# Performance work log

Hardware: AMD Instinct MI355X
Metric: run time of the kernel (lower is better)

## Reference

```python
import jax, jax.numpy as jnp
import numpy as np

CURV_BOUNDS = (-2.0, 2.0)
THRESH = 0.01   # |k| below this -> Euclidean branch
EPS = 1e-5

B, S, D = 4, 2048, 512


def setup_inputs() -> dict:
    key = jax.random.key(0)
    ks = jax.random.split(key, 8)
    x = jax.random.normal(ks[0], (B, S, D), jnp.float32)
    sc = 1.0 / np.sqrt(D)  # ~ nn.Linear default init scale
    Wq = jax.random.uniform(ks[1], (D, D), jnp.float32, -sc, sc)
    bq = jax.random.uniform(ks[2], (D,), jnp.float32, -sc, sc)
    Wk = jax.random.uniform(ks[3], (D, D), jnp.float32, -sc, sc)
    bk = jax.random.uniform(ks[4], (D,), jnp.float32, -sc, sc)
    Wv = jax.random.uniform(ks[5], (D, D), jnp.float32, -sc, sc)
    bv = jax.random.uniform(ks[6], (D,), jnp.float32, -sc, sc)
    curvature_raw = jnp.float32(0.5)   # init_curvature
    temperature = jnp.float32(1.0)
    mask = jnp.triu(jnp.ones((S, S), dtype=bool), 1)  # causal: True = masked out
    return {"x": x, "Wq": Wq, "bq": bq, "Wk": Wk, "bk": bk, "Wv": Wv,
            "bv": bv, "curvature_raw": curvature_raw,
            "temperature": temperature, "mask": mask}


def _curvature(raw):
    k_min, k_max = CURV_BOUNDS
    return k_min + (k_max - k_min) * (jnp.tanh(raw) + 1.0) / 2.0


def _project(u, k):
    # project_to_manifold: identity (euclid), Poincare-ball clip (k<0), sphere renorm (k>0)
    n = jnp.sqrt(jnp.sum(u * u, axis=-1, keepdims=True) + 1e-12)
    absk = jnp.abs(k)
    sk = jnp.sqrt(jnp.maximum(absk, EPS))
    max_norm = (1.0 - 1e-3) / sk                      # ball radius 1/sqrt(|k|)
    u_hyp = u * jnp.minimum(1.0, max_norm / n)
    u_sph = u / (n * sk)                              # sphere radius 1/sqrt(k)
    return jnp.where(absk < THRESH, u, jnp.where(k < 0, u_hyp, u_sph))


def reference(x, Wq, bq, Wk, bk, Wv, bv, curvature_raw, temperature, mask):
    k = _curvature(curvature_raw)
    q = x @ Wq.T + bq
    kk = x @ Wk.T + bk
    v = x @ Wv.T + bv
    qm = _project(q, k)
    km = _project(kk, k)

    # pairwise quantities without materializing [B,S,S,D]
    dots = jnp.einsum('bid,bjd->bij', qm, km)         # [B,S,S]
    qn2 = jnp.sum(qm * qm, axis=-1)                   # [B,S]
    kn2 = jnp.sum(km * km, axis=-1)                   # [B,S]
    diff2 = jnp.maximum(qn2[:, :, None] + kn2[:, None, :] - 2.0 * dots, 0.0)

    absk = jnp.abs(k)
    sk = jnp.sqrt(jnp.maximum(absk, EPS))

    d_euc = jnp.sqrt(diff2 + 1e-12)
    # hyperbolic (Poincare ball, c=|k|): acosh(1 + 2c|x-y|^2 / ((1-c|x|^2)(1-c|y|^2))) / sqrt(c)
    denom = jnp.maximum((1.0 - absk * qn2)[:, :, None] * (1.0 - absk * kn2)[:, None, :], EPS)
    arg = 1.0 + 2.0 * absk * diff2 / denom
    d_hyp = jnp.arccosh(jnp.maximum(arg, 1.0 + 1e-7)) / sk
    # spherical (radius 1/sqrt(k)): arccos(k * <x,y>) / sqrt(k)
    cosang = jnp.clip(absk * dots, -1.0 + 1e-7, 1.0 - 1e-7)
    d_sph = jnp.arccos(cosang) / sk

    dist = jnp.where(absk < THRESH, d_euc, jnp.where(k < 0, d_hyp, d_sph))

    scores = -dist / (temperature + 1e-8)
    scores = jnp.where(mask[None, :, :], -jnp.inf, scores)
    attention = jax.nn.softmax(scores, axis=-1)       # [B,S,S]
    output = jnp.einsum('bij,bjd->bid', attention, v) # [B,S,D]
    return output, attention
```

## Files before the change

### kernel.cpp

```cpp
#include <hip/hip_runtime.h>
#include <hip/hip_bf16.h>
#include <math.h>

typedef unsigned short u16;
typedef float float4e __attribute__((ext_vector_type(4)));
typedef short short8 __attribute__((ext_vector_type(8)));
typedef unsigned short ushort8 __attribute__((ext_vector_type(8)));
typedef unsigned short u16x4 __attribute__((ext_vector_type(4)));

#define SEQ 2048
#define DIM 512
#define NB  4

__device__ __forceinline__ float bf2f(u16 h) {
    return __uint_as_float(((unsigned)h) << 16);
}
__device__ __forceinline__ u16 f2bf(float f) {
    __hip_bfloat16 h = __float2bfloat16(f);
    return *reinterpret_cast<u16*>(&h);
}
__device__ __forceinline__ float curv_of(float raw) {
    return -2.0f + 2.0f * (tanhf(raw) + 1.0f);
}
__device__ __forceinline__ void gl_lds16(const u16* g, u16* lds) {
    __builtin_amdgcn_global_load_lds(
        (const __attribute__((address_space(1))) unsigned int*)g,
        (__attribute__((address_space(3))) unsigned int*)lds, 16, 0, 0);
}

__global__ __launch_bounds__(256) void cvt_all_kernel(
    const float* __restrict__ x, const float* __restrict__ Wq,
    const float* __restrict__ Wk, const float* __restrict__ Wv,
    u16* __restrict__ x_bf, u16* __restrict__ Wcat,
    float* __restrict__ lsum, float* __restrict__ qn2r, float* __restrict__ kn2r)
{
    const int n_x = NB * SEQ * DIM, n_w = DIM * DIM;
    int gid = blockIdx.x * 256 + threadIdx.x;
    if (gid < NB * SEQ) { lsum[gid] = 0.f; qn2r[gid] = 0.f; kn2r[gid] = 0.f; }
    int i4 = gid * 4;
    if (i4 < n_x) {
        float4 v = *(const float4*)&x[i4];
        u16x4 h = {f2bf(v.x), f2bf(v.y), f2bf(v.z), f2bf(v.w)};
        *(u16x4*)&x_bf[i4] = h;
    } else if (i4 < n_x + 3 * n_w) {
        int j = i4 - n_x;
        const float* W = (j < n_w) ? Wq : (j < 2 * n_w ? Wk : Wv);
        int off = j % n_w;
        float4 v = *(const float4*)&W[off];
        u16x4 h = {f2bf(v.x), f2bf(v.y), f2bf(v.z), f2bf(v.w)};
        *(u16x4*)&Wcat[j] = h;
    }
}

__global__ __launch_bounds__(256, 2) void gemm_qkv_kernel(
    const u16* __restrict__ A, const u16* __restrict__ Bt,
    u16* __restrict__ qbuf, u16* __restrict__ kbuf, u16* __restrict__ vT,
    const float* __restrict__ bq, const float* __restrict__ bk, const float* __restrict__ bv,
    float* __restrict__ qn2r, float* __restrict__ kn2r)
{
    const int lda = 512, ldb = 512;
    int n = blockIdx.x;
    int xcd = n & 7, i = n >> 3;
    int bn = i % 12, bm = xcd + 8 * (i / 12);

    __shared__ __align__(16) u16 As[128 * 64];
    __shared__ __align__(16) u16 Bs[128 * 64];

    int t = threadIdx.x, wave = t >> 6, lane = t & 63;
    int wr = wave >> 1, wc = wave & 1;
    int lrow = lane & 15, quad = lane >> 4;
    int srow = lane >> 3, sc8 = lane & 7;

    const u16* Ab = A + (size_t)(bm * 128) * lda;
    const u16* Bb = Bt + (size_t)(bn * 128) * ldb;

    float4e acc[4][4];
#pragma unroll
    for (int i2 = 0; i2 < 4; i2++)
#pragma unroll
        for (int j = 0; j < 4; j++) acc[i2][j] = (float4e){0.f, 0.f, 0.f, 0.f};

    for (int kt = 0; kt < 8; ++kt) {
        int k0 = kt << 6;
        __syncthreads();
#pragma unroll
        for (int h = 0; h < 4; ++h) {
            int q = wave * 4 + h;
            int row = q * 8 + srow;
            int c = sc8 ^ (row & 7);
            gl_lds16(Ab + (size_t)row * lda + k0 + c * 8, &As[q * 512]);
            gl_lds16(Bb + (size_t)row * ldb + k0 + c * 8, &Bs[q * 512]);
        }
        __syncthreads();
#pragma unroll
        for (int kk = 0; kk < 2; ++kk) {
            short8 af[4], bfr[4];
#pragma unroll
            for (int im = 0; im < 4; im++) {
                int R = wr * 64 + im * 16 + lrow;
                af[im] = *(const short8*)&As[R * 64 + (((kk * 4 + quad) ^ (R & 7)) * 8)];
            }
#pragma unroll
            for (int in = 0; in < 4; in++) {
                int R = wc * 64 + in * 16 + lrow;
                bfr[in] = *(const short8*)&Bs[R * 64 + (((kk * 4 + quad) ^ (R & 7)) * 8)];
            }
#pragma unroll
            for (int im = 0; im < 4; im++)
#pragma unroll
                for (int in = 0; in < 4; in++)
                    acc[im][in] = __builtin_amdgcn_mfma_f32_16x16x32_bf16(af[im], bfr[in], acc[im][in], 0, 0, 0);
        }
    }

    int region = bn >> 2;
    float nsum[4][4];
#pragma unroll
    for (int im = 0; im < 4; im++)
#pragma unroll
        for (int r = 0; r < 4; r++) nsum[im][r] = 0.f;

#pragma unroll
    for (int in = 0; in < 4; in++) {
        int gj = bn * 128 + wc * 64 + in * 16 + lrow;
        float bias = (gj < 512) ? bq[gj] : (gj < 1024 ? bk[gj - 512] : bv[gj - 1024]);
#pragma unroll
        for (int im = 0; im < 4; im++) {
            int gi0 = bm * 128 + wr * 64 + im * 16 + quad * 4;
            u16x4 pack;
#pragma unroll
            for (int r = 0; r < 4; r++) {
                u16 hv = f2bf(acc[im][in][r] + bias);
                pack[r] = hv;
                if (region == 0) {
                    qbuf[(size_t)(gi0 + r) * 512 + gj] = hv;
                } else if (region == 1) {
                    kbuf[(size_t)(gi0 + r) * 512 + (gj - 512)] = hv;
                }
                if (region < 2) { float vv = bf2f(hv); nsum[im][r] += vv * vv; }
            }
            if (region == 2) {
                int bb = gi0 >> 11, s = gi0 & 2047;
                *(u16x4*)&vT[((size_t)bb * DIM + (gj - 1024)) * SEQ + s] = pack;
            }
        }
    }
    if (region < 2) {
        float* nrm = (region == 0) ? qn2r : kn2r;
#pragma unroll
        for (int im = 0; im < 4; im++)
#pragma unroll
            for (int r = 0; r < 4; r++) {
                float v = nsum[im][r];
                v += __shfl_xor(v, 1);
                v += __shfl_xor(v, 2);
                v += __shfl_xor(v, 4);
                v += __shfl_xor(v, 8);
                if (lrow == 0)
                    atomicAdd(&nrm[bm * 128 + wr * 64 + im * 16 + quad * 4 + r], v);
            }
    }
}

__global__ __launch_bounds__(256) void rownorm_kernel(
    const float* __restrict__ qn2r, const float* __restrict__ kn2r,
    float2* __restrict__ qpk, float2* __restrict__ kpk,
    const float* __restrict__ curvp)
{
    int i = blockIdx.x * 256 + threadIdx.x;
    float kv = curv_of(curvp[0]);
    float absk = fabsf(kv);
    float sk = sqrtf(fmaxf(absk, 1e-5f));
    bool euc = (absk < 0.01f);
    float mxn = (1.0f - 1e-3f) / sk;

    float qr = qn2r[i];
    float nq = sqrtf(qr + 1e-12f);
    float sq_ = euc ? 1.f : (kv < 0.f ? fminf(1.f, mxn / nq) : 1.f / (nq * sk));
    qpk[i] = make_float2(qr * sq_ * sq_, sq_);

    float kr = kn2r[i];
    float nk = sqrtf(kr + 1e-12f);
    float sk_ = euc ? 1.f : (kv < 0.f ? fminf(1.f, mxn / nk) : 1.f / (nk * sk));
    kpk[i] = make_float2(kr * sk_ * sk_, sk_);
}

__global__ __launch_bounds__(256, 2) void gemm_scores_kernel(
    const u16* __restrict__ qbuf, const u16* __restrict__ kbuf,
    u16* __restrict__ attnH, float* __restrict__ lsum,
    const float2* __restrict__ qpk, const float2* __restrict__ kpk,
    const float* __restrict__ curvp, const float* __restrict__ tempp)
{
    const int lda = 512, ldb = 512, ldc = SEQ;
    int n = blockIdx.x;
    int xcd = n & 7, i = n >> 3;
    int bn = i & 15;
    int strip = xcd + 8 * (i >> 4);
    int bm = strip & 15, b = strip >> 4;
    if (bn > bm) return;

    __shared__ __align__(16) u16 As[128 * 64];
    __shared__ __align__(16) u16 Bs[128 * 64];

    int t = threadIdx.x, wave = t >> 6, lane = t & 63;
    int wr = wave >> 1, wc = wave & 1;
    int lrow = lane & 15, quad = lane >> 4;
    int srow = lane >> 3, sc8 = lane & 7;

    const u16* Ab = qbuf + (size_t)(b * SEQ + bm * 128) * lda;
    const u16* Bb = kbuf + (size_t)(b * SEQ + bn * 128) * ldb;

    float4e acc[4][4];
#pragma unroll
    for (int i2 = 0; i2 < 4; i2++)
#pragma unroll
        for (int j = 0; j < 4; j++) acc[i2][j] = (float4e){0.f, 0.f, 0.f, 0.f};

    for (int kt = 0; kt < 8; ++kt) {
        int k0 = kt << 6;
        __syncthreads();
#pragma unroll
        for (int h = 0; h < 4; ++h) {
            int q = wave * 4 + h;
            int row = q * 8 + srow;
            int c = sc8 ^ (row & 7);
            gl_lds16(Ab + (size_t)row * lda + k0 + c * 8, &As[q * 512]);
            gl_lds16(Bb + (size_t)row * ldb + k0 + c * 8, &Bs[q * 512]);
        }
        __syncthreads();
#pragma unroll
        for (int kk = 0; kk < 2; ++kk) {
            short8 af[4], bfr[4];
#pragma unroll
            for (int im = 0; im < 4; im++) {
                int R = wr * 64 + im * 16 + lrow;
                af[im] = *(const short8*)&As[R * 64 + (((kk * 4 + quad) ^ (R & 7)) * 8)];
            }
#pragma unroll
            for (int in = 0; in < 4; in++) {
                int R = wc * 64 + in * 16 + lrow;
                bfr[in] = *(const short8*)&Bs[R * 64 + (((kk * 4 + quad) ^ (R & 7)) * 8)];
            }
#pragma unroll
            for (int im = 0; im < 4; im++)
#pragma unroll
                for (int in = 0; in < 4; in++)
                    acc[im][in] = __builtin_amdgcn_mfma_f32_16x16x32_bf16(af[im], bfr[in], acc[im][in], 0, 0, 0);
        }
    }

    float kv = curv_of(curvp[0]);
    float absk = fabsf(kv);
    float sk = sqrtf(fmaxf(absk, 1e-5f));
    bool euc = (absk < 0.01f);
    float invT = 1.0f / (tempp[0] + 1e-8f);
    float Cexp = -1.4426950408889634f * invT;
    u16* Cb = attnH + (size_t)b * SEQ * SEQ;

    float2 kp[4];
#pragma unroll
    for (int in = 0; in < 4; in++)
        kp[in] = kpk[b * SEQ + bn * 128 + wc * 64 + in * 16 + lrow];

    float psum[4][4];
#pragma unroll
    for (int im = 0; im < 4; im++)
#pragma unroll
        for (int r = 0; r < 4; r++) psum[im][r] = 0.f;

#pragma unroll
    for (int im = 0; im < 4; im++) {
#pragma unroll
        for (int r = 0; r < 4; r++) {
            int gi = bm * 128 + wr * 64 + im * 16 + quad * 4 + r;
            float2 qp = qpk[b * SEQ + gi];
            float qn = qp.x;
#pragma unroll
            for (int in = 0; in < 4; in++) {
                int gj = bn * 128 + wc * 64 + in * 16 + lrow;
                float kn = kp[in].x;
                float dot = acc[im][in][r] * qp.y * kp[in].y;
                float diff2 = fmaxf(qn + kn - 2.f * dot, 0.f);
                float dist;
                if (euc) {
                    dist = sqrtf(diff2 + 1e-12f);
                } else if (kv < 0.f) {
                    float denom = fmaxf((1.f - absk * qn) * (1.f - absk * kn), 1e-5f);
                    float arg = fmaxf(1.f + 2.f * absk * diff2 / denom, 1.f + 1e-7f);
                    dist = acoshf(arg) / sk;
                } else {
                    float c = fminf(fmaxf(absk * dot, -1.f + 1e-7f), 1.f - 1e-7f);
                    dist = acosf(c) / sk;
                }
                float e = (gj <= gi) ? exp2f(dist * Cexp) : 0.f;
                Cb[(size_t)gi * ldc + gj] = f2bf(e);
                psum[im][r] += e;
            }
        }
    }
#pragma unroll
    for (int im = 0; im < 4; im++)
#pragma unroll
        for (int r = 0; r < 4; r++) {
            float v = psum[im][r];
            v += __shfl_xor(v, 1);
            v += __shfl_xor(v, 2);
            v += __shfl_xor(v, 4);
            v += __shfl_xor(v, 8);
            if (lrow == 0) {
                int gi = bm * 128 + wr * 64 + im * 16 + quad * 4 + r;
                atomicAdd(&lsum[b * SEQ + gi], v);
            }
        }
}

__global__ __launch_bounds__(256, 4) void gemm_pv_kernel(
    const u16* __restrict__ attnH, const u16* __restrict__ vT,
    float* __restrict__ out, float* __restrict__ attnF,
    const float* __restrict__ lsum)
{
    const int lda = SEQ, ldb = SEQ, ldc = DIM;
    int n = blockIdx.x;
    int xcd = n & 7, i = n >> 3;
    int bn = i & 7;
    int strip = xcd + 8 * (i >> 3);
    int bm = strip & 31, b = strip >> 5;

    __shared__ __align__(16) u16 As[64 * 64];
    __shared__ __align__(16) u16 Bs[64 * 64];

    int t = threadIdx.x, wave = t >> 6, lane = t & 63;
    int wr = wave >> 1, wc = wave & 1;
    int lrow = lane & 15, quad = lane >> 4;
    int srow = lane >> 3, sc = lane & 7;

    const u16* Ab = attnH + (size_t)b * SEQ * SEQ + (size_t)(bm * 64) * lda;
    const u16* Bb = vT + (size_t)b * DIM * SEQ + (size_t)(bn * 64) * ldb;
    float* attnFb = attnF + (size_t)b * SEQ * SEQ;

    {
        int r = t >> 2, c4 = t & 3;
        float4 z = (float4){0.f, 0.f, 0.f, 0.f};
        for (int kt = bm + 1; kt < 32; ++kt)
            if ((kt & 7) == bn) {
                float* dst = attnFb + (size_t)(bm * 64 + r) * SEQ + kt * 64 + c4 * 16;
                ((float4*)dst)[0] = z; ((float4*)dst)[1] = z;
                ((float4*)dst)[2] = z; ((float4*)dst)[3] = z;
            }
    }

    float4e acc[2][2];
#pragma unroll
    for (int i2 = 0; i2 < 2; i2++)
#pragma unroll
        for (int j = 0; j < 2; j++) acc[i2][j] = (float4e){0.f, 0.f, 0.f, 0.f};

    for (int kt = 0; kt <= bm; ++kt) {
        int k0 = kt << 6;
        __syncthreads();
#pragma unroll
        for (int h = 0; h < 2; ++h) {
            int q = wave * 2 + h;
            int row = q * 8 + srow;
            int c = sc ^ (row & 7);
            gl_lds16(Ab + (size_t)row * lda + k0 + c * 8, &As[q * 512]);
            gl_lds16(Bb + (size_t)row * ldb + k0 + c * 8, &Bs[q * 512]);
        }
        __syncthreads();
#pragma unroll
        for (int s = 0; s < 2; ++s) {
            short8 af[2], bfr[2];
#pragma unroll
            for (int im = 0; im < 2; im++) {
                int R = wr * 32 + im * 16 + lrow;
                af[im] = *(const short8*)&As[R * 64 + (((s * 4 + quad) ^ (R & 7)) * 8)];
            }
#pragma unroll
            for (int in = 0; in < 2; in++) {
                int R = wc * 32 + in * 16 + lrow;
                bfr[in] = *(const short8*)&Bs[R * 64 + (((s * 4 + quad) ^ (R & 7)) * 8)];
            }
#pragma unroll
            for (int im = 0; im < 2; im++)
#pragma unroll
                for (int in = 0; in < 2; in++)
                    acc[im][in] = __builtin_amdgcn_mfma_f32_16x16x32_bf16(af[im], bfr[in], acc[im][in], 0, 0, 0);
        }
        if ((kt & 7) == bn) {
            int r = t >> 2, c4 = t & 3;
            int gi = bm * 64 + r;
            float invl = 1.0f / lsum[b * SEQ + gi];
            const u16* src = &As[r * 64];
            int j0 = c4 * 2;
            ushort8 u0 = *(const ushort8*)&src[(j0 ^ (r & 7)) * 8];
            ushort8 u1 = *(const ushort8*)&src[((j0 + 1) ^ (r & 7)) * 8];
            float* dst = attnFb + (size_t)gi * SEQ + kt * 64 + c4 * 16;
            float4 f0 = {bf2f(u0[0]) * invl, bf2f(u0[1]) * invl, bf2f(u0[2]) * invl, bf2f(u0[3]) * invl};
            float4 f1 = {bf2f(u0[4]) * invl, bf2f(u0[5]) * invl, bf2f(u0[6]) * invl, bf2f(u0[7]) * invl};
            float4 f2 = {bf2f(u1[0]) * invl, bf2f(u1[1]) * invl, bf2f(u1[2]) * invl, bf2f(u1[3]) * invl};
            float4 f3 = {bf2f(u1[4]) * invl, bf2f(u1[5]) * invl, bf2f(u1[6]) * invl, bf2f(u1[7]) * invl};
            ((float4*)dst)[0] = f0; ((float4*)dst)[1] = f1;
            ((float4*)dst)[2] = f2; ((float4*)dst)[3] = f3;
        }
    }

    float* Cb = out + (size_t)b * SEQ * DIM;
#pragma unroll
    for (int im = 0; im < 2; im++)
#pragma unroll
        for (int r = 0; r < 4; r++) {
            int gi = bm * 64 + wr * 32 + im * 16 + quad * 4 + r;
            float invl = 1.0f / lsum[b * SEQ + gi];
#pragma unroll
            for (int in = 0; in < 2; in++) {
                int gd = bn * 64 + wc * 32 + in * 16 + lrow;
                Cb[(size_t)gi * ldc + gd] = acc[im][in][r] * invl;
            }
        }
}

extern "C" void kernel_launch(void* const* d_in, const int* in_sizes, int n_in,
                              void* d_out, int out_size, void* d_ws, size_t ws_size,
                              hipStream_t stream) {
    (void)in_sizes; (void)n_in; (void)out_size; (void)ws_size;

    const float* x    = (const float*)d_in[0];
    const float* Wq   = (const float*)d_in[1];
    const float* bq   = (const float*)d_in[2];
    const float* Wk   = (const float*)d_in[3];
    const float* bk   = (const float*)d_in[4];
    const float* Wv   = (const float*)d_in[5];
    const float* bv   = (const float*)d_in[6];
    const float* curv = (const float*)d_in[7];
    const float* temp = (const float*)d_in[8];

    float* out   = (float*)d_out;
    float* attnF = out + (size_t)NB * SEQ * DIM;

    char* ws = (char*)d_ws;
    u16*   x_bf  = (u16*)(ws + 0);
    u16*   Wcat  = (u16*)(ws + 8388608);
    u16*   attnH = (u16*)(ws + 0);
    u16*   qbuf  = (u16*)(ws + 33554432);
    u16*   kbuf  = (u16*)(ws + 41943040);
    u16*   vT    = (u16*)(ws + 50331648);
    float* qn2r  = (float*)(ws + 58720256);
    float* kn2r  = (float*)(ws + 58753024);
    float* lsum  = (float*)(ws + 58785792);
    float2* qpk  = (float2*)(ws + 58818560);
    float2* kpk  = (float2*)(ws + 58884096);

    {
        int n_tot = (NB * SEQ * DIM + 3 * DIM * DIM) / 4;
        cvt_all_kernel<<<(n_tot + 255) / 256, 256, 0, stream>>>(
            x, Wq, Wk, Wv, x_bf, Wcat, lsum, qn2r, kn2r);
    }

    gemm_qkv_kernel<<<768, 256, 0, stream>>>(
        x_bf, Wcat, qbuf, kbuf, vT, bq, bk, bv, qn2r, kn2r);

    rownorm_kernel<<<NB * SEQ / 256, 256, 0, stream>>>(qn2r, kn2r, qpk, kpk, curv);

    gemm_scores_kernel<<<1024, 256, 0, stream>>>(
        qbuf, kbuf, attnH, lsum, qpk, kpk, curv, temp);

    gemm_pv_kernel<<<1024, 256, 0, stream>>>(
        attnH, vT, out, attnF, lsum);
}
```

Measured before the change: 234.0 us.

## Double-buffer LDS tiles with async prefetch in all three GEMM kernels

Each GEMM kernel (QKV projection, scores, PV) now keeps two LDS buffers and issues the global-to-LDS loads for the next K tile before computing the current one. It waits on a partial vmcnt so the newest loads stay in flight, and syncs with explicit barriers. The aim is to hide global load latency behind MFMA work. In exchange LDS use doubles, which can lower occupancy for the launch_bounds(256,4) PV kernel. Correctness also now depends on the hand-set vmcnt values matching the number of loads issued per stage.

```diff
diff --git a/kernel.cpp b/kernel.cpp
--- a/kernel.cpp
+++ b/kernel.cpp
@@ -11,6 +11,9 @@
 #define SEQ 2048
 #define DIM 512
 #define NB  4
+
+#define VMCNT(n) asm volatile("s_waitcnt vmcnt(" #n ")" ::: "memory")
+#define BAR() __builtin_amdgcn_s_barrier()
 
 __device__ __forceinline__ float bf2f(u16 h) {
     return __uint_as_float(((unsigned)h) << 16);
@@ -63,8 +66,8 @@
     int xcd = n & 7, i = n >> 3;
     int bn = i % 12, bm = xcd + 8 * (i / 12);
 
-    __shared__ __align__(16) u16 As[128 * 64];
-    __shared__ __align__(16) u16 Bs[128 * 64];
+    __shared__ __align__(16) u16 As[2][128 * 64];
+    __shared__ __align__(16) u16 Bs[2][128 * 64];
 
     int t = threadIdx.x, wave = t >> 6, lane = t & 63;
     int wr = wave >> 1, wc = wave & 1;
@@ -74,36 +77,42 @@
     const u16* Ab = A + (size_t)(bm * 128) * lda;
     const u16* Bb = Bt + (size_t)(bn * 128) * ldb;
 
-    float4e acc[4][4];
-#pragma unroll
-    for (int i2 = 0; i2 < 4; i2++)
-#pragma unroll
-        for (int j = 0; j < 4; j++) acc[i2][j] = (float4e){0.f, 0.f, 0.f, 0.f};
-
-    for (int kt = 0; kt < 8; ++kt) {
+    auto stage = [&](int buf, int kt) {
         int k0 = kt << 6;
-        __syncthreads();
 #pragma unroll
         for (int h = 0; h < 4; ++h) {
             int q = wave * 4 + h;
             int row = q * 8 + srow;
             int c = sc8 ^ (row & 7);
-            gl_lds16(Ab + (size_t)row * lda + k0 + c * 8, &As[q * 512]);
-            gl_lds16(Bb + (size_t)row * ldb + k0 + c * 8, &Bs[q * 512]);
-        }
-        __syncthreads();
+            gl_lds16(Ab + (size_t)row * lda + k0 + c * 8, &As[buf][q * 512]);
+            gl_lds16(Bb + (size_t)row * ldb + k0 + c * 8, &Bs[buf][q * 512]);
+        }
+    };
+
+    float4e acc[4][4];
+#pragma unroll
+    for (int i2 = 0; i2 < 4; i2++)
+#pragma unroll
+        for (int j = 0; j < 4; j++) acc[i2][j] = (float4e){0.f, 0.f, 0.f, 0.f};
+
+    stage(0, 0);
+    for (int kt = 0; kt < 8; ++kt) {
+        int cur = kt & 1;
+        if (kt + 1 < 8) { stage(cur ^ 1, kt + 1); VMCNT(8); }
+        else            { VMCNT(0); }
+        BAR();
 #pragma unroll
         for (int kk = 0; kk < 2; ++kk) {
             short8 af[4], bfr[4];
 #pragma unroll
             for (int im = 0; im < 4; im++) {
                 int R = wr * 64 + im * 16 + lrow;
-                af[im] = *(const short8*)&As[R * 64 + (((kk * 4 + quad) ^ (R & 7)) * 8)];
+                af[im] = *(const short8*)&As[cur][R * 64 + (((kk * 4 + quad) ^ (R & 7)) * 8)];
             }
 #pragma unroll
             for (int in = 0; in < 4; in++) {
                 int R = wc * 64 + in * 16 + lrow;
-                bfr[in] = *(const short8*)&Bs[R * 64 + (((kk * 4 + quad) ^ (R & 7)) * 8)];
+                bfr[in] = *(const short8*)&Bs[cur][R * 64 + (((kk * 4 + quad) ^ (R & 7)) * 8)];
             }
 #pragma unroll
             for (int im = 0; im < 4; im++)
@@ -111,6 +120,7 @@
                 for (int in = 0; in < 4; in++)
                     acc[im][in] = __builtin_amdgcn_mfma_f32_16x16x32_bf16(af[im], bfr[in], acc[im][in], 0, 0, 0);
         }
+        BAR();
     }
 
     int region = bn >> 2;
@@ -199,8 +209,8 @@
     int bm = strip & 15, b = strip >> 4;
     if (bn > bm) return;
 
-    __shared__ __align__(16) u16 As[128 * 64];
-    __shared__ __align__(16) u16 Bs[128 * 64];
+    __shared__ __align__(16) u16 As[2][128 * 64];
+    __shared__ __align__(16) u16 Bs[2][128 * 64];
 
     int t = threadIdx.x, wave = t >> 6, lane = t & 63;
     int wr = wave >> 1, wc = wave & 1;
@@ -210,36 +220,42 @@
     const u16* Ab = qbuf + (size_t)(b * SEQ + bm * 128) * lda;
     const u16* Bb = kbuf + (size_t)(b * SEQ + bn * 128) * ldb;
 
-    float4e acc[4][4];
-#pragma unroll
-    for (int i2 = 0; i2 < 4; i2++)
-#pragma unroll
-        for (int j = 0; j < 4; j++) acc[i2][j] = (float4e){0.f, 0.f, 0.f, 0.f};
-
-    for (int kt = 0; kt < 8; ++kt) {
+    auto stage = [&](int buf, int kt) {
         int k0 = kt << 6;
-        __syncthreads();
 #pragma unroll
         for (int h = 0; h < 4; ++h) {
             int q = wave * 4 + h;
             int row = q * 8 + srow;
             int c = sc8 ^ (row & 7);
-            gl_lds16(Ab + (size_t)row * lda + k0 + c * 8, &As[q * 512]);
-            gl_lds16(Bb + (size_t)row * ldb + k0 + c * 8, &Bs[q * 512]);
-        }
-        __syncthreads();
+            gl_lds16(Ab + (size_t)row * lda + k0 + c * 8, &As[buf][q * 512]);
+            gl_lds16(Bb + (size_t)row * ldb + k0 + c * 8, &Bs[buf][q * 512]);
+        }
+    };
+
+    float4e acc[4][4];
+#pragma unroll
+    for (int i2 = 0; i2 < 4; i2++)
+#pragma unroll
+        for (int j = 0; j < 4; j++) acc[i2][j] = (float4e){0.f, 0.f, 0.f, 0.f};
+
+    stage(0, 0);
+    for (int kt = 0; kt < 8; ++kt) {
+        int cur = kt & 1;
+        if (kt + 1 < 8) { stage(cur ^ 1, kt + 1); VMCNT(8); }
+        else            { VMCNT(0); }
+        BAR();
 #pragma unroll
         for (int kk = 0; kk < 2; ++kk) {
             short8 af[4], bfr[4];
 #pragma unroll
             for (int im = 0; im < 4; im++) {
                 int R = wr * 64 + im * 16 + lrow;
-                af[im] = *(const short8*)&As[R * 64 + (((kk * 4 + quad) ^ (R & 7)) * 8)];
+                af[im] = *(const short8*)&As[cur][R * 64 + (((kk * 4 + quad) ^ (R & 7)) * 8)];
             }
 #pragma unroll
             for (int in = 0; in < 4; in++) {
                 int R = wc * 64 + in * 16 + lrow;
-                bfr[in] = *(const short8*)&Bs[R * 64 + (((kk * 4 + quad) ^ (R & 7)) * 8)];
+                bfr[in] = *(const short8*)&Bs[cur][R * 64 + (((kk * 4 + quad) ^ (R & 7)) * 8)];
             }
 #pragma unroll
             for (int im = 0; im < 4; im++)
@@ -247,6 +263,7 @@
                 for (int in = 0; in < 4; in++)
                     acc[im][in] = __builtin_amdgcn_mfma_f32_16x16x32_bf16(af[im], bfr[in], acc[im][in], 0, 0, 0);
         }
+        BAR();
     }
 
     float kv = curv_of(curvp[0]);
@@ -326,8 +343,8 @@
     int strip = xcd + 8 * (i >> 3);
     int bm = strip & 31, b = strip >> 5;
 
-    __shared__ __align__(16) u16 As[64 * 64];
-    __shared__ __align__(16) u16 Bs[64 * 64];
+    __shared__ __align__(16) u16 As[2][64 * 64];
+    __shared__ __align__(16) u16 Bs[2][64 * 64];
 
     int t = threadIdx.x, wave = t >> 6, lane = t & 63;
     int wr = wave >> 1, wc = wave & 1;
@@ -349,36 +366,42 @@
             }
     }
 
-    float4e acc[2][2];
-#pragma unroll
-    for (int i2 = 0; i2 < 2; i2++)
-#pragma unroll
-        for (int j = 0; j < 2; j++) acc[i2][j] = (float4e){0.f, 0.f, 0.f, 0.f};
-
-    for (int kt = 0; kt <= bm; ++kt) {
+    auto stage = [&](int buf, int kt) {
         int k0 = kt << 6;
-        __syncthreads();
 #pragma unroll
         for (int h = 0; h < 2; ++h) {
             int q = wave * 2 + h;
             int row = q * 8 + srow;
             int c = sc ^ (row & 7);
-            gl_lds16(Ab + (size_t)row * lda + k0 + c * 8, &As[q * 512]);
-            gl_lds16(Bb + (size_t)row * ldb + k0 + c * 8, &Bs[q * 512]);
-        }
-        __syncthreads();
+            gl_lds16(Ab + (size_t)row * lda + k0 + c * 8, &As[buf][q * 512]);
+            gl_lds16(Bb + (size_t)row * ldb + k0 + c * 8, &Bs[buf][q * 512]);
+        }
+    };
+
+    float4e acc[2][2];
+#pragma unroll
+    for (int i2 = 0; i2 < 2; i2++)
+#pragma unroll
+        for (int j = 0; j < 2; j++) acc[i2][j] = (float4e){0.f, 0.f, 0.f, 0.f};
+
+    stage(0, 0);
+    for (int kt = 0; kt <= bm; ++kt) {
+        int cur = kt & 1;
+        if (kt < bm) { stage(cur ^ 1, kt + 1); VMCNT(4); }
+        else         { VMCNT(0); }
+        BAR();
 #pragma unroll
         for (int s = 0; s < 2; ++s) {
             short8 af[2], bfr[2];
 #pragma unroll
             for (int im = 0; im < 2; im++) {
                 int R = wr * 32 + im * 16 + lrow;
-                af[im] = *(const short8*)&As[R * 64 + (((s * 4 + quad) ^ (R & 7)) * 8)];
+                af[im] = *(const short8*)&As[cur][R * 64 + (((s * 4 + quad) ^ (R & 7)) * 8)];
             }
 #pragma unroll
             for (int in = 0; in < 2; in++) {
                 int R = wc * 32 + in * 16 + lrow;
-                bfr[in] = *(const short8*)&Bs[R * 64 + (((s * 4 + quad) ^ (R & 7)) * 8)];
+                bfr[in] = *(const short8*)&Bs[cur][R * 64 + (((s * 4 + quad) ^ (R & 7)) * 8)];
             }
 #pragma unroll
             for (int im = 0; im < 2; im++)
@@ -390,7 +413,7 @@
             int r = t >> 2, c4 = t & 3;
             int gi = bm * 64 + r;
             float invl = 1.0f / lsum[b * SEQ + gi];
-            const u16* src = &As[r * 64];
+            const u16* src = &As[cur][r * 64];
             int j0 = c4 * 2;
             ushort8 u0 = *(const ushort8*)&src[(j0 ^ (r & 7)) * 8];
             ushort8 u1 = *(const ushort8*)&src[((j0 + 1) ^ (r & 7)) * 8];
@@ -402,6 +425,7 @@
             ((float4*)dst)[0] = f0; ((float4*)dst)[1] = f1;
             ((float4*)dst)[2] = f2; ((float4*)dst)[3] = f3;
         }
+        BAR();
     }
 
     float* Cb = out + (size_t)b * SEQ * DIM;
```

Result: slower. 276.6 us (+18.2%).
